# Kernel tuning notes

Hardware: AMD Instinct MI355X
Metric: run time of the kernel (lower is better)

Reference implementation:

```python
import jax, jax.numpy as jnp
import numpy as np

B, C, V = 1024, 512, 256  # batch, num_conjunctions, num_variables


def setup_inputs() -> dict:
    key = jax.random.key(0)
    k1, k2, k3 = jax.random.split(key, 3)
    x0 = jax.random.uniform(k1, (B, V), dtype=jnp.float32)
    # torch init: conj = 1 - 2*rand  -> uniform in (-1, 1)
    conjunctions = 1.0 - 2.0 * jax.random.uniform(k2, (C, 2 * V), dtype=jnp.float32)
    # rw = 10 - 20*rand -> uniform in (-10, 10)
    rule_weights = 10.0 - 20.0 * jax.random.uniform(k3, (C,), dtype=jnp.float32)
    return {"x0": x0, "conjunctions": conjunctions, "rule_weights": rule_weights}


def reference(x0, conjunctions, rule_weights):
    mu = jax.nn.sigmoid(conjunctions)            # (C, 2V)
    x = jnp.concatenate((x0, 1.0 - x0), axis=1)  # (B, 2V)
    # fuzzy-AND: broadcast mul-add then min over literal axis
    x_pot = mu[None, :, :] * x[:, None, :] + (1.0 - mu)[None, :, :]  # (B, C, 2V)
    fit = jnp.min(x_pot, axis=-1)                # (B, C)
    return 5.0 + jnp.sum(rule_weights * fit, axis=-1)  # (B,)
```

## Files before the change

kernel.cpp:

```cpp
#include <hip/hip_runtime.h>


#define B_    1024
#define C_    512
#define V_    256
#define TWOV  512

#define CPW    128
#define NCHUNK (C_ / CPW)
#define BPB    8
#define NBG    (B_ / BPB)
#define WAVES  8
#define VPW    32
#define HVP    8

__global__ __launch_bounds__(256) void k_prep(const float* __restrict__ conj,
                                              float2* __restrict__ muT2,
                                              float* __restrict__ out) {
    const int c = blockIdx.x;
    const int v = threadIdx.x;
    if (c < 4) out[c * 256 + v] = 5.0f;
    float z1 = conj[(size_t)c * TWOV + v];
    float z2 = conj[(size_t)c * TWOV + V_ + v];
    float m1 = 1.0f / (1.0f + __expf(-z1));
    float m2 = 1.0f / (1.0f + __expf(-z2));
    muT2[(size_t)(v >> 1) * (2 * C_) + c * 2 + (v & 1)] = make_float2(m1, m2);
}

__global__ __launch_bounds__(512, 4) void k_main(const float* __restrict__ x0,
                                                 const float4* __restrict__ muT4,
                                                 const float* __restrict__ rw,
                                                 float* __restrict__ out) {
    const int tid   = threadIdx.x;
    const int lane  = tid & 63;
    const int wave  = tid >> 6;
    const int chunk = blockIdx.y;
    const int cA    = chunk * CPW + lane;
    const int cB    = cA + 64;
    const int bg    = blockIdx.x;
    const int v0    = wave * VPW;

    __shared__ float4 xs[BPB * V_ / 4];
    __shared__ float  red[2 * BPB * WAVES * 64];

    {
        const float4* xg = reinterpret_cast<const float4*>(x0 + (size_t)bg * BPB * V_);
        xs[tid] = xg[tid];
    }

    const float4* mup = muT4 + (size_t)(v0 >> 1) * C_ + cA;

    float mA[BPB], mB[BPB];
#pragma unroll
    for (int i = 0; i < BPB; ++i) { mA[i] = 0.0f; mB[i] = 0.0f; }

    __syncthreads();

#pragma unroll
    for (int h = 0; h < 2; ++h) {
        float4 mrA[HVP], mrB[HVP];
#pragma unroll
        for (int p = 0; p < HVP; ++p) {
            mrA[p] = mup[(size_t)(h * HVP + p) * C_];
            mrB[p] = mup[(size_t)(h * HVP + p) * C_ + 64];
        }
#pragma unroll
        for (int p = 0; p < HVP; ++p) {
            asm volatile("" : "+v"(mrA[p].x), "+v"(mrA[p].y), "+v"(mrA[p].z), "+v"(mrA[p].w));
            asm volatile("" : "+v"(mrB[p].x), "+v"(mrB[p].y), "+v"(mrB[p].z), "+v"(mrB[p].w));
        }

#pragma unroll
        for (int bi = 0; bi < BPB; ++bi) {
            const int xb = bi * (V_ / 4) + (v0 >> 2) + h * 4;
            float4 xa = xs[xb + 0];
            float4 xc = xs[xb + 1];
            float4 xd = xs[xb + 2];
            float4 xe = xs[xb + 3];
            float ma = mA[bi], mb = mB[bi];
#define STEP(P, XA, XB) \
            ma = fmaxf(ma, fmaxf(__builtin_fmaf(-mrA[P].x, (XA), mrA[P].x), mrA[P].y * (XA))); \
            ma = fmaxf(ma, fmaxf(__builtin_fmaf(-mrA[P].z, (XB), mrA[P].z), mrA[P].w * (XB))); \
            mb = fmaxf(mb, fmaxf(__builtin_fmaf(-mrB[P].x, (XA), mrB[P].x), mrB[P].y * (XA))); \
            mb = fmaxf(mb, fmaxf(__builtin_fmaf(-mrB[P].z, (XB), mrB[P].z), mrB[P].w * (XB)));
            STEP(0, xa.x, xa.y)  STEP(1, xa.z, xa.w)
            STEP(2, xc.x, xc.y)  STEP(3, xc.z, xc.w)
            STEP(4, xd.x, xd.y)  STEP(5, xd.z, xd.w)
            STEP(6, xe.x, xe.y)  STEP(7, xe.z, xe.w)
#undef STEP
            mA[bi] = ma; mB[bi] = mb;
        }
    }

#pragma unroll
    for (int bi = 0; bi < BPB; ++bi) {
        red[bi * (WAVES * 64) + tid] = mA[bi];
        red[(BPB + bi) * (WAVES * 64) + tid] = mB[bi];
    }
    __syncthreads();

    float ma = red[wave * (WAVES * 64) + lane];
    float mb = red[(BPB + wave) * (WAVES * 64) + lane];
#pragma unroll
    for (int k = 1; k < WAVES; ++k) {
        ma = fmaxf(ma, red[wave * (WAVES * 64) + k * 64 + lane]);
        mb = fmaxf(mb, red[(BPB + wave) * (WAVES * 64) + k * 64 + lane]);
    }
    float s = rw[cA] * (1.0f - ma) + rw[cB] * (1.0f - mb);
    s += __shfl_xor(s, 1, 64);
    s += __shfl_xor(s, 2, 64);
    s += __shfl_xor(s, 4, 64);
    s += __shfl_xor(s, 8, 64);
    s += __shfl_xor(s, 16, 64);
    s += __shfl_xor(s, 32, 64);
    if (lane == 0)
        atomicAdd(&out[bg * BPB + wave], s);
}

__global__ __launch_bounds__(256) void k_naive(const float* __restrict__ x0,
                                               const float* __restrict__ conj,
                                               const float* __restrict__ rw,
                                               float* __restrict__ out) {
    int b = blockIdx.x;
    int t = threadIdx.x;
    __shared__ float red[256];
    float acc = 0.0f;
    for (int c = t; c < C_; c += 256) {
        float m = 0.0f;
        for (int v = 0; v < V_; ++v) {
            float mu1 = 1.0f / (1.0f + expf(-conj[(size_t)c * TWOV + v]));
            float mu2 = 1.0f / (1.0f + expf(-conj[(size_t)c * TWOV + V_ + v]));
            float x = x0[(size_t)b * V_ + v];
            m = fmaxf(m, fmaxf(mu1 * (1.0f - x), mu2 * x));
        }
        acc += rw[c] * (1.0f - m);
    }
    red[t] = acc;
    __syncthreads();
    for (int s = 128; s > 0; s >>= 1) {
        if (t < s) red[t] += red[t + s];
        __syncthreads();
    }
    if (t == 0) out[b] = 5.0f + red[0];
}

extern "C" void kernel_launch(void* const* d_in, const int* in_sizes, int n_in,
                              void* d_out, int out_size, void* d_ws, size_t ws_size,
                              hipStream_t stream) {
    const float* x0   = (const float*)d_in[0];
    const float* conj = (const float*)d_in[1];
    const float* rw   = (const float*)d_in[2];
    float* out = (float*)d_out;

    const size_t mu_floats = (size_t)(V_ / 2) * C_ * 4;
    const size_t need = mu_floats * sizeof(float);

    if (ws_size < need) {
        k_naive<<<B_, 256, 0, stream>>>(x0, conj, rw, out);
        return;
    }

    float4* muT4 = (float4*)d_ws;

    k_prep<<<C_, 256, 0, stream>>>(conj, (float2*)muT4, out);
    dim3 grid(NBG, NCHUNK);
    k_main<<<grid, 512, 0, stream>>>(x0, muT4, rw, out);
}
```

Baseline: 23.83 us.

## Software-pipeline mu loads two stages ahead of compute in k_main

Replaces the two-half structure, which loaded all 16 float4 mu values per half and then computed, with an 8-stage loop. Each stage consumes 4 float4s and issues the loads for the stage two steps ahead. It also issues the x0 global load and the first mu loads before the shared-memory store and barrier, so their latency overlaps the barrier. The aim is to hide global-memory latency behind compute, at the cost of finer-grained dependencies and more live registers.

```diff
diff --git a/kernel.cpp b/kernel.cpp
--- a/kernel.cpp
+++ b/kernel.cpp
@@ -12,7 +12,7 @@
 #define NBG    (B_ / BPB)
 #define WAVES  8
 #define VPW    32
-#define HVP    8
+#define NE     8
 
 __global__ __launch_bounds__(256) void k_prep(const float* __restrict__ conj,
                                               float2* __restrict__ muT2,
@@ -43,54 +43,58 @@
     __shared__ float4 xs[BPB * V_ / 4];
     __shared__ float  red[2 * BPB * WAVES * 64];
 
-    {
-        const float4* xg = reinterpret_cast<const float4*>(x0 + (size_t)bg * BPB * V_);
-        xs[tid] = xg[tid];
-    }
+    const float4* xg = reinterpret_cast<const float4*>(x0 + (size_t)bg * BPB * V_);
+    float4 xv = xg[tid];
 
     const float4* mup = muT4 + (size_t)(v0 >> 1) * C_ + cA;
+
+    float4 A[NE][2], Bv[NE][2];
+#define ISSUE(q) do { \
+        A[q][0]  = mup[(size_t)(2*(q)    ) * C_]; \
+        A[q][1]  = mup[(size_t)(2*(q) + 1) * C_]; \
+        Bv[q][0] = mup[(size_t)(2*(q)    ) * C_ + 64]; \
+        Bv[q][1] = mup[(size_t)(2*(q) + 1) * C_ + 64]; \
+    } while (0)
+#define PINq(q) do { \
+        asm volatile("" : "+v"(A[q][0].x),  "+v"(A[q][0].y),  "+v"(A[q][0].z),  "+v"(A[q][0].w), \
+                          "+v"(A[q][1].x),  "+v"(A[q][1].y),  "+v"(A[q][1].z),  "+v"(A[q][1].w)); \
+        asm volatile("" : "+v"(Bv[q][0].x), "+v"(Bv[q][0].y), "+v"(Bv[q][0].z), "+v"(Bv[q][0].w), \
+                          "+v"(Bv[q][1].x), "+v"(Bv[q][1].y), "+v"(Bv[q][1].z), "+v"(Bv[q][1].w)); \
+    } while (0)
+
+    ISSUE(0);
+    ISSUE(1);
 
     float mA[BPB], mB[BPB];
 #pragma unroll
     for (int i = 0; i < BPB; ++i) { mA[i] = 0.0f; mB[i] = 0.0f; }
 
+    xs[tid] = xv;
     __syncthreads();
 
-#pragma unroll
-    for (int h = 0; h < 2; ++h) {
-        float4 mrA[HVP], mrB[HVP];
-#pragma unroll
-        for (int p = 0; p < HVP; ++p) {
-            mrA[p] = mup[(size_t)(h * HVP + p) * C_];
-            mrB[p] = mup[(size_t)(h * HVP + p) * C_ + 64];
-        }
-#pragma unroll
-        for (int p = 0; p < HVP; ++p) {
-            asm volatile("" : "+v"(mrA[p].x), "+v"(mrA[p].y), "+v"(mrA[p].z), "+v"(mrA[p].w));
-            asm volatile("" : "+v"(mrB[p].x), "+v"(mrB[p].y), "+v"(mrB[p].z), "+v"(mrB[p].w));
-        }
+    const int xbase = v0 >> 2;
 
 #pragma unroll
+    for (int q = 0; q < NE; ++q) {
+        PINq(q);
+        if (q + 2 < NE) ISSUE(q + 2);
+#pragma unroll
         for (int bi = 0; bi < BPB; ++bi) {
-            const int xb = bi * (V_ / 4) + (v0 >> 2) + h * 4;
-            float4 xa = xs[xb + 0];
-            float4 xc = xs[xb + 1];
-            float4 xd = xs[xb + 2];
-            float4 xe = xs[xb + 3];
+            float4 xc = xs[bi * (V_ / 4) + xbase + q];
             float ma = mA[bi], mb = mB[bi];
-#define STEP(P, XA, XB) \
-            ma = fmaxf(ma, fmaxf(__builtin_fmaf(-mrA[P].x, (XA), mrA[P].x), mrA[P].y * (XA))); \
-            ma = fmaxf(ma, fmaxf(__builtin_fmaf(-mrA[P].z, (XB), mrA[P].z), mrA[P].w * (XB))); \
-            mb = fmaxf(mb, fmaxf(__builtin_fmaf(-mrB[P].x, (XA), mrB[P].x), mrB[P].y * (XA))); \
-            mb = fmaxf(mb, fmaxf(__builtin_fmaf(-mrB[P].z, (XB), mrB[P].z), mrB[P].w * (XB)));
-            STEP(0, xa.x, xa.y)  STEP(1, xa.z, xa.w)
-            STEP(2, xc.x, xc.y)  STEP(3, xc.z, xc.w)
-            STEP(4, xd.x, xd.y)  STEP(5, xd.z, xd.w)
-            STEP(6, xe.x, xe.y)  STEP(7, xe.z, xe.w)
-#undef STEP
+            ma = fmaxf(ma, fmaxf(__builtin_fmaf(-A[q][0].x, xc.x, A[q][0].x),  A[q][0].y  * xc.x));
+            ma = fmaxf(ma, fmaxf(__builtin_fmaf(-A[q][0].z, xc.y, A[q][0].z),  A[q][0].w  * xc.y));
+            ma = fmaxf(ma, fmaxf(__builtin_fmaf(-A[q][1].x, xc.z, A[q][1].x),  A[q][1].y  * xc.z));
+            ma = fmaxf(ma, fmaxf(__builtin_fmaf(-A[q][1].z, xc.w, A[q][1].z),  A[q][1].w  * xc.w));
+            mb = fmaxf(mb, fmaxf(__builtin_fmaf(-Bv[q][0].x, xc.x, Bv[q][0].x), Bv[q][0].y * xc.x));
+            mb = fmaxf(mb, fmaxf(__builtin_fmaf(-Bv[q][0].z, xc.y, Bv[q][0].z), Bv[q][0].w * xc.y));
+            mb = fmaxf(mb, fmaxf(__builtin_fmaf(-Bv[q][1].x, xc.z, Bv[q][1].x), Bv[q][1].y * xc.z));
+            mb = fmaxf(mb, fmaxf(__builtin_fmaf(-Bv[q][1].z, xc.w, Bv[q][1].z), Bv[q][1].w * xc.w));
             mA[bi] = ma; mB[bi] = mb;
         }
     }
+#undef ISSUE
+#undef PINq
 
 #pragma unroll
     for (int bi = 0; bi < BPB; ++bi) {
```

After: 27.22 us. 14.2% more time.
